# Optimization experiments

Measured on AMD Instinct MI355X. Metric: run time of the kernel, lower is better.

## Reference

```python
import jax, jax.numpy as jnp
from jax import lax
import numpy as np


def _conv3d(x, W, b, stride=1, pad=1):
    y = lax.conv_general_dilated(x, W, (stride,) * 3, [(pad, pad)] * 3,
                                 dimension_numbers=('NCDHW', 'OIDHW', 'NCDHW'))
    return y + b[None, :, None, None, None]


def _deconv3d(x, W, b):
    # PyTorch ConvTranspose3d(k=4, s=2, p=1) == conv with lhs_dilation=2,
    # per-side pad = k-1-p = 2, spatially flipped kernel; W is (Cin, Cout, 4,4,4).
    Wf = jnp.flip(W, axis=(2, 3, 4)).transpose(1, 0, 2, 3, 4)
    y = lax.conv_general_dilated(x, Wf, (1, 1, 1), [(2, 2)] * 3,
                                 lhs_dilation=(2, 2, 2),
                                 dimension_numbers=('NCDHW', 'OIDHW', 'NCDHW'))
    return y + b[None, :, None, None, None]


def _inorm(x, eps=1e-5):
    # InstanceNorm3d (affine=False): normalize per (B, C) over spatial dims
    m = jnp.mean(x, axis=(2, 3, 4), keepdims=True)
    v = jnp.var(x, axis=(2, 3, 4), keepdims=True)
    return (x - m) * lax.rsqrt(v + eps)


def _leaky(x):
    return jnp.where(x >= 0, x, 0.1 * x)


def _cblock(x, W, b, stride=1):
    return _leaky(_inorm(_conv3d(x, W, b, stride)))


def _cost_volume(f1, f2, r=2):
    # Faithful to the original pad/mul/crop loop:
    # cost[shift][p] = mean_c f1[c, p] * f2[c, p + shift], zero-padded OOB.
    B, C, D, H, W = f1.shape
    f2p = jnp.pad(f2, ((0, 0), (0, 0), (r, r), (r, r), (r, r)))
    cv = [jnp.mean(f1 * f2p[:, :, r + v:r + v + D, r + h:r + h + H, r + d:r + d + W], axis=1)
          for v in range(-r, r + 1)
          for h in range(-r, r + 1)
          for d in range(-r, r + 1)]
    return jnp.stack(cv, axis=1)  # (B, (2r+1)^3 = 125, D, H, W)


def _warp(img, flow):
    # SpatialTransformation: dense 3D warp, trilinear sample at grid + flow,
    # coordinates clamped to the volume border.
    B, C, D, H, W = img.shape
    gd, gh, gw = jnp.meshgrid(jnp.arange(D, dtype=img.dtype),
                              jnp.arange(H, dtype=img.dtype),
                              jnp.arange(W, dtype=img.dtype), indexing='ij')
    cd = jnp.clip(gd[None] + flow[:, 0], 0.0, D - 1.0)
    ch = jnp.clip(gh[None] + flow[:, 1], 0.0, H - 1.0)
    cw = jnp.clip(gw[None] + flow[:, 2], 0.0, W - 1.0)

    def samp_b(imb, d, h, w):
        return jax.vmap(lambda c: jax.scipy.ndimage.map_coordinates(
            c, [d, h, w], order=1, mode='nearest'))(imb)

    return jax.vmap(samp_b)(img, cd, ch, cw)


def _forward(atlas, target, W_ct, b_ct, W1a, b1a, W1aa, b1aa, W1b, b1b,
             W2a, b2a, W2aa, b2aa, W2b, b2b,
             W20, b20, Wpf2, bpf2, Wd2, bd2, Wuf2, buf2,
             W10, b10, Wpf1, bpf1, Wd1, bd1, Wuf1, buf1,
             W00, b00, Wpf0, bpf0, Wd0, bd0):
    # modality='CT' (shared CT encoder), G=True, contrastive=False path
    im2 = _cblock(atlas, W_ct, b_ct, stride=2)
    im1 = _cblock(target, W_ct, b_ct, stride=2)
    c11 = _cblock(_cblock(_cblock(im1, W1a, b1a, 2), W1aa, b1aa), W1b, b1b)
    c21 = _cblock(_cblock(_cblock(im2, W1a, b1a, 2), W1aa, b1aa), W1b, b1b)
    c12 = _cblock(_cblock(_cblock(c11, W2a, b2a, 2), W2aa, b2aa), W2b, b2b)
    c22 = _cblock(_cblock(_cblock(c21, W2a, b2a, 2), W2aa, b2aa), W2b, b2b)

    x = _leaky(_cost_volume(c12, c22))
    x = _cblock(x, W20, b20)
    flow2 = _conv3d(x, Wpf2, bpf2)
    up_flow2 = _deconv3d(flow2, Wd2, bd2)
    up_feat2 = _deconv3d(x, Wuf2, buf2)

    warp1 = _warp(c21, up_flow2)
    corr1 = _leaky(_cost_volume(c11, warp1))
    x = jnp.concatenate((corr1, c11, up_flow2, up_feat2), axis=1)  # 125+16+3+3=147
    x = _cblock(x, W10, b10)
    flow1 = _conv3d(x, Wpf1, bpf1)
    up_flow1 = _deconv3d(flow1, Wd1, bd1)
    up_feat1 = _deconv3d(x, Wuf1, buf1)

    warp0 = _warp(im2, up_flow1)
    corr0 = _leaky(_cost_volume(im1, warp0))
    x = jnp.concatenate((corr0, im1, up_flow1, up_feat1), axis=1)  # 125+4+3+64=196
    x = _cblock(x, W00, b00)
    flow0 = _conv3d(x, Wpf0, bpf0)
    flow = _deconv3d(flow0, Wd0, bd0)
    return flow, c22, c12


def setup_inputs() -> dict:
    ks = jax.random.split(jax.random.key(0), 24)

    def w(i, shape):
        fan_in = int(np.prod(shape[1:]))
        return jax.random.normal(ks[i], shape, jnp.float32) * np.float32(np.sqrt(2.0 / fan_in))

    z = lambda n: jnp.zeros((n,), jnp.float32)
    S = 128
    return {
        'atlas': jax.random.normal(ks[0], (1, 1, S, S, S), jnp.float32),
        'target': jax.random.normal(ks[1], (1, 1, S, S, S), jnp.float32),
        'W_ct': w(2, (4, 1, 3, 3, 3)), 'b_ct': z(4),
        'W1a': w(3, (16, 4, 3, 3, 3)), 'b1a': z(16),
        'W1aa': w(4, (16, 16, 3, 3, 3)), 'b1aa': z(16),
        'W1b': w(5, (16, 16, 3, 3, 3)), 'b1b': z(16),
        'W2a': w(6, (32, 16, 3, 3, 3)), 'b2a': z(32),
        'W2aa': w(7, (32, 32, 3, 3, 3)), 'b2aa': z(32),
        'W2b': w(8, (32, 32, 3, 3, 3)), 'b2b': z(32),
        'W20': w(9, (32, 125, 3, 3, 3)), 'b20': z(32),
        'Wpf2': w(10, (3, 32, 3, 3, 3)) * 0.1, 'bpf2': z(3),
        'Wd2': w(11, (3, 3, 4, 4, 4)), 'bd2': z(3),
        'Wuf2': w(12, (32, 3, 4, 4, 4)), 'buf2': z(3),
        'W10': w(13, (32, 147, 3, 3, 3)), 'b10': z(32),
        'Wpf1': w(14, (3, 32, 3, 3, 3)) * 0.1, 'bpf1': z(3),
        'Wd1': w(15, (3, 3, 4, 4, 4)), 'bd1': z(3),
        'Wuf1': w(16, (32, 64, 4, 4, 4)), 'buf1': z(64),
        'W00': w(17, (32, 196, 3, 3, 3)), 'b00': z(32),
        'Wpf0': w(18, (3, 32, 3, 3, 3)) * 0.1, 'bpf0': z(3),
        'Wd0': w(19, (3, 3, 4, 4, 4)), 'bd0': z(3),
    }


def reference(atlas, target, W_ct, b_ct, W1a, b1a, W1aa, b1aa, W1b, b1b,
              W2a, b2a, W2aa, b2aa, W2b, b2b,
              W20, b20, Wpf2, bpf2, Wd2, bd2, Wuf2, buf2,
              W10, b10, Wpf1, bpf1, Wd1, bd1, Wuf1, buf1,
              W00, b00, Wpf0, bpf0, Wd0, bd0):
    return _forward(atlas, target, W_ct, b_ct, W1a, b1a, W1aa, b1aa, W1b, b1b,
                    W2a, b2a, W2aa, b2aa, W2b, b2b,
                    W20, b20, Wpf2, bpf2, Wd2, bd2, Wuf2, buf2,
                    W10, b10, Wpf1, bpf1, Wd1, bd1, Wuf1, buf1,
                    W00, b00, Wpf0, bpf0, Wd0, bd0)
```

## Files before the change

kernel.cpp:

```cpp
#include <hip/hip_runtime.h>
#include <cstddef>
#include <cstdint>

#define DIVUP(a,b) (((a)+(b)-1)/(b))

typedef __attribute__((ext_vector_type(8))) short short8;
typedef __attribute__((ext_vector_type(4))) float f32x4;

__device__ __forceinline__ ushort f2bf(float f) {
    union { float f; uint32_t u; } v; v.f = f;
    uint32_t r = v.u + 0x7fffu + ((v.u >> 16) & 1u);
    return (ushort)(r >> 16);
}

struct SwzB { int x, y, z; };
__device__ __forceinline__ SwzB swz_block() {
    int gx = gridDim.x, gy = gridDim.y;
    int n = gx * gy * gridDim.z;
    int lin = blockIdx.x + gx * (blockIdx.y + gy * blockIdx.z);
    if ((n & 7) == 0)
        lin = (lin & 7) * (n >> 3) + (lin >> 3);
    SwzB s;
    s.x = lin % gx;
    int t = lin / gx;
    s.y = t % gy;
    s.z = t / gy;
    return s;
}

template<int COUT, int STRIDE>
__global__ __launch_bounds__(256)
void conv3x3_k(const float* __restrict__ in0, const float* __restrict__ in1,
               const float* __restrict__ wgt, const float* __restrict__ bias,
               float* __restrict__ out, float* __restrict__ stats,
               int Cin, int D, int H, int W, int nz, long out_bs, int st_bs)
{
    constexpr int TD = 4, TH = 8, TW = 8;
    constexpr int ID = 2 * TD + 1, IH = 2 * TH + 1, IW = 2 * TW + 1;
    __shared__ float tile[ID * IH * IW];
    const int b = blockIdx.z / nz, zb = blockIdx.z % nz;
    const float* in = b ? in1 : in0;
    out += (long)b * out_bs;
    if (stats) stats += 2 * st_bs * b;
    const int Do = D / STRIDE, Ho = H / STRIDE, Wo = W / STRIDE;
    const int tid = threadIdx.x;
    const int tw = tid & 7, th = (tid >> 3) & 7, td = tid >> 6;
    const int ow0 = blockIdx.x * TW, oh0 = blockIdx.y * TH, od0 = zb * TD;
    const int iw0 = ow0 * STRIDE - 1, ih0 = oh0 * STRIDE - 1, id0 = od0 * STRIDE - 1;
    const size_t HWs = (size_t)H * W;

    float acc[COUT];
#pragma unroll
    for (int i = 0; i < COUT; i++) acc[i] = 0.f;

    for (int c = 0; c < Cin; ++c) {
        const float* inc = in + (size_t)c * D * HWs;
        for (int i = tid; i < ID * IH * IW; i += 256) {
            int lw = i % IW, lh = (i / IW) % IH, ld = i / (IW * IH);
            int gw = iw0 + lw, gh = ih0 + lh, gd = id0 + ld;
            float v = 0.f;
            if ((unsigned)gw < (unsigned)W && (unsigned)gh < (unsigned)H &&
                (unsigned)gd < (unsigned)D)
                v = inc[(size_t)gd * HWs + (size_t)gh * W + gw];
            tile[i] = v;
        }
        __syncthreads();
        float r[27];
        const int bd = td * STRIDE, bh = th * STRIDE, bw = tw * STRIDE;
#pragma unroll
        for (int kd = 0; kd < 3; kd++)
#pragma unroll
            for (int kh = 0; kh < 3; kh++)
#pragma unroll
                for (int kw = 0; kw < 3; kw++)
                    r[kd * 9 + kh * 3 + kw] =
                        tile[(bd + kd) * (IH * IW) + (bh + kh) * IW + (bw + kw)];
#pragma unroll
        for (int oc = 0; oc < COUT; ++oc) {
            const float* wp = wgt + ((size_t)oc * Cin + c) * 27;
            float s = 0.f;
#pragma unroll
            for (int t = 0; t < 27; t++) s = fmaf(wp[t], r[t], s);
            acc[oc] += s;
        }
        __syncthreads();
    }
    const size_t So = (size_t)Do * Ho * Wo;
    const size_t sp = (size_t)(od0 + td) * Ho * Wo + (size_t)(oh0 + th) * Wo + (ow0 + tw);
#pragma unroll
    for (int oc = 0; oc < COUT; ++oc)
        out[(size_t)oc * So + sp] = acc[oc] + bias[oc];

    if (stats) {
        __syncthreads();
        float* sm = tile;
        const int wv = tid >> 6, l = tid & 63;
#pragma unroll
        for (int oc = 0; oc < COUT; ++oc) {
            float sv = acc[oc] + bias[oc];
            float sq = sv * sv;
#pragma unroll
            for (int o = 32; o > 0; o >>= 1) {
                sv += __shfl_down(sv, o, 64);
                sq += __shfl_down(sq, o, 64);
            }
            if (l == 0) { sm[(wv * COUT + oc) * 2] = sv; sm[(wv * COUT + oc) * 2 + 1] = sq; }
        }
        __syncthreads();
        if (tid < COUT) {
            float s = 0.f, s2 = 0.f;
#pragma unroll
            for (int w = 0; w < 4; ++w) {
                s += sm[(w * COUT + tid) * 2];
                s2 += sm[(w * COUT + tid) * 2 + 1];
            }
            atomicAdd(&stats[2 * tid], s);
            atomicAdd(&stats[2 * tid + 1], s2);
        }
    }
}

template<int CP, int NF, int STRIDE, int MW, int COUTR>
__global__ __launch_bounds__(MW * 64, (STRIDE == 1) ? 2 : 4)
void mconv_k(const ushort* __restrict__ xcl, const ushort* __restrict__ wp,
             const float* __restrict__ bias, float* __restrict__ outcf,
             float* __restrict__ stats, const ushort* __restrict__ zbuf,
             int D, int H, int W, int nz, long in_bs, long out_bs, int st_bs)
{
    constexpr int KC = CP / 32;
    constexpr int MF = (STRIDE == 1) ? 4 : 1;
    constexpr int TD = MW;
    constexpr int TWl = (STRIDE == 1) ? 8 : 4;
    constexpr int HD = (STRIDE == 1) ? TD + 2 : 2 * TD + 1;
    constexpr int HH = (STRIDE == 1) ? 10 : 9;
    constexpr int HWd = (STRIDE == 1) ? 10 : 9;
    constexpr int HALO = HD * HH * HWd;
    constexpr int NTH = MW * 64;
    constexpr int NIT = (HALO * 4 + NTH - 1) / NTH;
    constexpr int PITCH = (STRIDE == 1) ? 32 : 40;
    constexpr bool WLDS = (STRIDE == 1);
    constexpr int LDSZ_H = (STRIDE == 1) ? NIT * NTH * 8 : HALO * 40;
    constexpr int NITW = (9 * NF * 512 + NTH * 8 - 1) / (NTH * 8);
    constexpr int LDSZ_W = NITW * NTH * 8;
    constexpr int LDS_TOT = WLDS ? LDSZ_H + 2 * LDSZ_W : LDSZ_H;
    __shared__ __align__(16) ushort lds[LDS_TOT];

    const int tid = threadIdx.x;
    const int wv = tid >> 6, l = tid & 63;
    const SwzB sb = swz_block();
    const int b = sb.z / nz, zb = sb.z % nz;
    xcl += (long)b * in_bs;
    outcf += (long)b * out_bs;
    if (stats) stats += 2 * st_bs * b;
    const int od0 = zb * TD, oh0 = sb.y * ((STRIDE == 1) ? 8 : 4),
              ow0 = sb.x * TWl;
    const int id0 = od0 * STRIDE - 1, ih0 = oh0 * STRIDE - 1, iw0 = ow0 * STRIDE - 1;

    f32x4 acc[MF][NF];
#pragma unroll
    for (int mf = 0; mf < MF; mf++)
#pragma unroll
        for (int nf = 0; nf < NF; nf++) acc[mf][nf] = f32x4{0.f, 0.f, 0.f, 0.f};

    auto woff = [&](int kc, int kd, int kh, int kw, int nf) -> size_t {
        return ((((size_t)(kc * 3 + kd) * 3 + kh) * 3 + kw) * NF + nf) << 9;
    };

    if constexpr (WLDS) {
        ushort* const hab = lds;
        ushort* const wbA = lds + LDSZ_H;
        ushort* const wbB = lds + LDSZ_H + LDSZ_W;

        auto hstage = [&](int kc) {
#pragma unroll
            for (int it = 0; it < NIT; ++it) {
                int idx = it * NTH + tid;
                int pt = idx >> 2, part = idx & 3;
                int lw = pt % HWd, lh = (pt / HWd) % HH, ld = pt / (HWd * HH);
                int gx = iw0 + lw, gy = ih0 + lh, gz = id0 + ld;
                const ushort* src = zbuf;
                if (pt < HALO && (unsigned)gx < (unsigned)W &&
                    (unsigned)gy < (unsigned)H && (unsigned)gz < (unsigned)D)
                    src = xcl + (size_t)((gz * H + gy) * W + gx) * CP + part * 8;
                __builtin_amdgcn_global_load_lds(
                    (const __attribute__((address_space(1))) uint32_t*)(src + kc * 32),
                    (__attribute__((address_space(3))) uint32_t*)
                        &hab[(size_t)(it * NTH + (wv << 6)) * 8],
                    16, 0, 0);
            }
        };
        auto wstage = [&](int kc, int kd, ushort* dst) {
#pragma unroll
            for (int it = 0; it < NITW; ++it) {
                int idx = it * NTH + tid;
                const ushort* src = (idx < 9 * NF * 64)
                    ? wp + ((size_t)(kc * 3 + kd) * 9 * NF * 512 + (size_t)idx * 8)
                    : zbuf;
                __builtin_amdgcn_global_load_lds(
                    (const __attribute__((address_space(1))) uint32_t*)src,
                    (__attribute__((address_space(3))) uint32_t*)
                        &dst[(size_t)(it * NTH + (wv << 6)) * 8],
                    16, 0, 0);
            }
        };
        auto compute = [&](int kd, const ushort* w) {
#pragma unroll
            for (int kw = 0; kw < 3; ++kw) {
                short8 af[9];
#pragma unroll
                for (int r = 0; r < 9; ++r)
                    af[r] = *reinterpret_cast<const short8*>(
                        &hab[((wv + kd) * (HH * HWd) +
                              (r + ((l >> 3) & 1)) * HWd + (l & 7) + kw) * PITCH +
                             ((l >> 4) << 3)]);
#pragma unroll
                for (int kh = 0; kh < 3; ++kh) {
                    short8 bf[NF];
#pragma unroll
                    for (int nf = 0; nf < NF; ++nf)
                        bf[nf] = *reinterpret_cast<const short8*>(
                            &w[(size_t)(((kh * 3 + kw) * NF) + nf) * 512 + (l << 3)]);
#pragma unroll
                    for (int mf = 0; mf < MF; ++mf)
#pragma unroll
                        for (int nf = 0; nf < NF; ++nf)
                            acc[mf][nf] = __builtin_amdgcn_mfma_f32_16x16x32_bf16(
                                af[2 * mf + kh], bf[nf], acc[mf][nf], 0, 0, 0);
                }
            }
        };

        for (int kc = 0; kc < KC; ++kc) {
            hstage(kc);
            wstage(kc, 0, wbA);
            __syncthreads();
            wstage(kc, 1, wbB);
            compute(0, wbA);
            __syncthreads();
            wstage(kc, 2, wbA);
            compute(1, wbB);
            __syncthreads();
            compute(2, wbA);
            __syncthreads();
        }
    } else {
        uint4 v[NIT];
        auto stage = [&](int kc) {
#pragma unroll
            for (int it = 0; it < NIT; ++it) {
                int idx = it * NTH + tid;
                uint4 t = {0u, 0u, 0u, 0u};
                if (idx < HALO * 4) {
                    int pt = idx >> 2, part = idx & 3;
                    int lw = pt % HWd, lh = (pt / HWd) % HH, ld = pt / (HWd * HH);
                    int gx = iw0 + lw, gy = ih0 + lh, gz = id0 + ld;
                    if ((unsigned)gx < (unsigned)W && (unsigned)gy < (unsigned)H &&
                        (unsigned)gz < (unsigned)D)
                        t = *reinterpret_cast<const uint4*>(
                            xcl + ((size_t)((gz * H + gy) * W + gx)) * CP + kc * 32 + part * 8);
                }
                v[it] = t;
            }
        };

        stage(0);
        for (int kc = 0; kc < KC; ++kc) {
            if (kc) __syncthreads();
#pragma unroll
            for (int it = 0; it < NIT; ++it) {
                int idx = it * NTH + tid;
                if (idx < HALO * 4)
                    *reinterpret_cast<uint4*>(&lds[(idx >> 2) * PITCH + (idx & 3) * 8]) = v[it];
            }
            __syncthreads();
            if (kc + 1 < KC) stage(kc + 1);
#pragma unroll
            for (int t = 0; t < 27; ++t) {
                const int kd = t / 9, kh = (t / 3) % 3, kw = t % 3;
                short8 bf[NF];
#pragma unroll
                for (int nf = 0; nf < NF; ++nf)
                    bf[nf] = *reinterpret_cast<const short8*>(
                        wp + woff(kc, kd, kh, kw, nf) + (l << 3));
                int bw = l & 3, bh = (l >> 2) & 3;
                int p_loc = (2 * wv + kd) * (HH * HWd) + (2 * bh + kh) * HWd + (2 * bw + kw);
                short8 afs = *reinterpret_cast<const short8*>(&lds[p_loc * PITCH + ((l >> 4) << 3)]);
#pragma unroll
                for (int nf = 0; nf < NF; ++nf)
                    acc[0][nf] = __builtin_amdgcn_mfma_f32_16x16x32_bf16(
                        afs, bf[nf], acc[0][nf], 0, 0, 0);
            }
        }
    }
    const int Do = D / STRIDE, Ho = H / STRIDE, Wo = W / STRIDE;
    const size_t So = (size_t)Do * Ho * Wo;
    float ps[NF], ps2[NF];
#pragma unroll
    for (int nf = 0; nf < NF; ++nf) { ps[nf] = 0.f; ps2[nf] = 0.f; }
#pragma unroll
    for (int nf = 0; nf < NF; ++nf) {
        int oc = nf * 16 + (l & 15);
        float bv = (oc < COUTR) ? bias[oc] : 0.f;
#pragma unroll
        for (int mf = 0; mf < MF; ++mf) {
#pragma unroll
            for (int r = 0; r < 4; ++r) {
                int q = ((l >> 4) << 2) + r;
                int bw, bh;
                if (STRIDE == 1) { bw = q & 7; bh = 2 * mf + (q >> 3); }
                else             { bw = q & 3; bh = (q >> 2) & 3; }
                int p = ((od0 + wv) * Ho + (oh0 + bh)) * Wo + (ow0 + bw);
                float val = acc[mf][nf][r] + bv;
                if (oc < COUTR) {
                    outcf[(size_t)oc * So + p] = val;
                    ps[nf] += val; ps2[nf] = fmaf(val, val, ps2[nf]);
                }
            }
        }
    }
    if (stats) {
        __syncthreads();
        float* sm = (float*)lds;
#pragma unroll
        for (int nf = 0; nf < NF; ++nf) {
            float s = ps[nf], s2 = ps2[nf];
            s += __shfl_down(s, 32, 64);  s2 += __shfl_down(s2, 32, 64);
            s += __shfl_down(s, 16, 64);  s2 += __shfl_down(s2, 16, 64);
            if (l < 16) {
                sm[((wv * NF + nf) * 16 + l) * 2] = s;
                sm[((wv * NF + nf) * 16 + l) * 2 + 1] = s2;
            }
        }
        __syncthreads();
        if (tid < NF * 16) {
            int nf = tid >> 4, c = tid & 15, oc = nf * 16 + c;
            if (oc < COUTR) {
                float s = 0.f, s2 = 0.f;
#pragma unroll
                for (int w = 0; w < MW; ++w) {
                    s += sm[((w * NF + nf) * 16 + c) * 2];
                    s2 += sm[((w * NF + nf) * 16 + c) * 2 + 1];
                }
                atomicAdd(&stats[2 * oc], s);
                atomicAdd(&stats[2 * oc + 1], s2);
            }
        }
    }
}

struct WTask { const float* src; void* dst; int kind, Cin, COUT, KC, coutr, base; };
struct WTab { WTask t[17]; int n; };

__global__ __launch_bounds__(256)
void wprep_k(WTab tab)
{
    int b = blockIdx.x, ti = 0;
    for (int i = 0; i < tab.n; ++i) if (b >= tab.t[i].base) ti = i;
    const WTask tk = tab.t[ti];
    int idx = (b - tk.base) * 256 + threadIdx.x;
    if (tk.kind == 0) {
        int NF = tk.COUT >> 4;
        int tot = 27 * tk.KC * NF * 512;
        if (idx >= tot) return;
        int j = idx & 7, l = (idx >> 3) & 63;
        int g = idx >> 9;
        int nf = g % NF; g /= NF;
        int kw = g % 3; g /= 3;
        int kh = g % 3; g /= 3;
        int kd = g % 3; int kc = g / 3;
        int t = kd * 9 + kh * 3 + kw;
        int oc = nf * 16 + (l & 15);
        int c = kc * 32 + ((l >> 4) << 3) + j;
        float v = (c < tk.Cin && oc < tk.coutr)
                      ? tk.src[((size_t)oc * tk.Cin + c) * 27 + t] : 0.f;
        ((ushort*)tk.dst)[idx] = f2bf(v);
    } else if (tk.kind == 1) {
        int NF = tk.KC;
        int tot = 8 * 8 * NF * 512;
        if (idx >= tot) return;
        int j = idx & 7, l = (idx >> 3) & 63;
        int g = idx >> 9;
        int nf = g % NF; g /= NF;
        int t = g % 8; int pp = g / 8;
        int oc = nf * 16 + (l & 15);
        int c = ((l >> 4) << 3) + j;
        int kd_ = (t >> 2) & 1, kh_ = (t >> 1) & 1, kw_ = t & 1;
        int pd = (pp >> 2) & 1, ph = (pp >> 1) & 1, pw = pp & 1;
        int kd = 3 - pd - 2 * kd_, kh = 3 - ph - 2 * kh_, kw = 3 - pw - 2 * kw_;
        float v = (oc < tk.COUT)
                      ? tk.src[(size_t)(c * tk.COUT + oc) * 64 + kd * 16 + kh * 4 + kw] : 0.f;
        ((ushort*)tk.dst)[idx] = f2bf(v);
    } else {
        int tot = tk.Cin * tk.COUT * 64;
        if (idx >= tot) return;
        int k = idx & 63; int oc = (idx >> 6) % tk.COUT; int c = (idx >> 6) / tk.COUT;
        ((float*)tk.dst)[((size_t)c * 64 + k) * tk.COUT + oc] = tk.src[idx];
    }
}

template<int NF>
__global__ __launch_bounds__(256)
void mdeconv_k(const ushort* __restrict__ xcl, const ushort* __restrict__ wpd,
               const float* __restrict__ bias, ushort* __restrict__ outcl,
               int c0, int CPo, int Si)
{
    constexpr int HD = 5, HH = 9, HWd = 9, HALO = HD * HH * HWd;
    constexpr int PITCH = 32;
    __shared__ __align__(16) ushort lds[HALO * PITCH];
    const int tid = threadIdx.x, wv = tid >> 6, l = tid & 63;
    const SwzB sb = swz_block();
    const int pp = sb.z & 7, tz = sb.z >> 3;
    const int pd = (pp >> 2) & 1, ph = (pp >> 1) & 1, pw = pp & 1;
    const int oz0 = tz * 4, oy0 = sb.y * 8, ox0 = sb.x * 8;
    const int iz0 = oz0 + pd - 1, iy0 = oy0 + ph - 1, ix0 = ox0 + pw - 1;

    for (int idx = tid; idx < HALO * 4; idx += 256) {
        int pt = idx >> 2, part = idx & 3;
        int lw = pt % HWd, lh = (pt / HWd) % HH, ld = pt / (HWd * HH);
        int gx = ix0 + lw, gy = iy0 + lh, gz = iz0 + ld;
        uint4 t = {0u, 0u, 0u, 0u};
        if ((unsigned)gx < (unsigned)Si && (unsigned)gy < (unsigned)Si &&
            (unsigned)gz < (unsigned)Si)
            t = *reinterpret_cast<const uint4*>(
                xcl + ((size_t)((gz * Si + gy) * Si + gx)) * 32 + part * 8);
        *reinterpret_cast<uint4*>(&lds[pt * PITCH + part * 8]) = t;
    }
    __syncthreads();

    f32x4 acc[4][NF];
#pragma unroll
    for (int mf = 0; mf < 4; mf++)
#pragma unroll
        for (int nf = 0; nf < NF; nf++) acc[mf][nf] = f32x4{0.f, 0.f, 0.f, 0.f};

#pragma unroll
    for (int kd = 0; kd < 2; ++kd) {
#pragma unroll
        for (int kw = 0; kw < 2; ++kw) {
            short8 af[8];
#pragma unroll
            for (int r = 0; r < 8; ++r)
                af[r] = *reinterpret_cast<const short8*>(
                    &lds[((wv + kd) * (HH * HWd) + (r + ((l >> 3) & 1)) * HWd +
                          (l & 7) + kw) * PITCH + ((l >> 4) << 3)]);
#pragma unroll
            for (int kh = 0; kh < 2; ++kh) {
                const int t = kd * 4 + kh * 2 + kw;
                short8 bf[NF];
#pragma unroll
                for (int nf = 0; nf < NF; ++nf)
                    bf[nf] = *reinterpret_cast<const short8*>(
                        wpd + (((size_t)(pp * 8 + t) * NF + nf) << 9) + (l << 3));
#pragma unroll
                for (int mf = 0; mf < 4; ++mf)
#pragma unroll
                    for (int nf = 0; nf < NF; ++nf)
                        acc[mf][nf] = __builtin_amdgcn_mfma_f32_16x16x32_bf16(
                            af[2 * mf + kh], bf[nf], acc[mf][nf], 0, 0, 0);
            }
        }
    }
    const int Do = 2 * Si;
#pragma unroll
    for (int nf = 0; nf < NF; ++nf) {
        int oc = nf * 16 + (l & 15);
        float bv = bias[oc];
#pragma unroll
        for (int mf = 0; mf < 4; ++mf) {
#pragma unroll
            for (int r = 0; r < 4; ++r) {
                int q = ((l >> 4) << 2) + r;
                int bw = q & 7, bh = 2 * mf + (q >> 3);
                int oD = 2 * (oz0 + wv) + pd, oH = 2 * (oy0 + bh) + ph, oW = 2 * (ox0 + bw) + pw;
                outcl[(size_t)((oD * Do + oH) * Do + oW) * CPo + c0 + oc] =
                    f2bf(acc[mf][nf][r] + bv);
            }
        }
    }
}

template<int CIN>
__global__ __launch_bounds__(256)
void dctn_k(const float* __restrict__ in, const float* __restrict__ wt,
            const float* __restrict__ bias, float* __restrict__ outcf,
            ushort* __restrict__ outcl, int c0, int CPo, int Si)
{
    const int Do = 2 * Si;
    const size_t So = (size_t)Do * Do * Do, ni = (size_t)Si * Si * Si;
    size_t p = (size_t)blockIdx.x * 256 + threadIdx.x;
    if (p >= So) return;
    int oxW = (int)(p % Do), oyH = (int)((p / Do) % Do), ozD = (int)(p / ((size_t)Do * Do));
    int pw = oxW & 1, ph = oyH & 1, pd = ozD & 1;
    int xb = oxW >> 1, yb = oyH >> 1, zb = ozD >> 1;
    float acc[3] = {0.f, 0.f, 0.f};
    for (int c = 0; c < CIN; ++c) {
        const float* inc = in + (size_t)c * ni;
        const float* wc = wt + (size_t)c * 64 * 3;
#pragma unroll
        for (int jd = 0; jd < 2; jd++) {
            int iz = zb + pd - jd; if ((unsigned)iz >= (unsigned)Si) continue;
            int kd = 1 - pd + 2 * jd;
#pragma unroll
            for (int jh = 0; jh < 2; jh++) {
                int iy = yb + ph - jh; if ((unsigned)iy >= (unsigned)Si) continue;
                int kh = 1 - ph + 2 * jh;
#pragma unroll
                for (int jw = 0; jw < 2; jw++) {
                    int ix = xb + pw - jw; if ((unsigned)ix >= (unsigned)Si) continue;
                    int kw = 1 - pw + 2 * jw;
                    float v = inc[((size_t)iz * Si + iy) * Si + ix];
                    const float* wr = wc + (size_t)((kd * 4 + kh) * 4 + kw) * 3;
                    acc[0] = fmaf(wr[0], v, acc[0]);
                    acc[1] = fmaf(wr[1], v, acc[1]);
                    acc[2] = fmaf(wr[2], v, acc[2]);
                }
            }
        }
    }
#pragma unroll
    for (int oc = 0; oc < 3; ++oc) {
        float o = acc[oc] + bias[oc];
        if (outcf) outcf[(size_t)oc * So + p] = o;
        if (outcl) outcl[p * CPo + c0 + oc] = f2bf(o);
    }
}

__global__ __launch_bounds__(256)
void inorm_apply_k(const float* __restrict__ x, const float* __restrict__ stats,
                   float* __restrict__ y, size_t S, float invS,
                   ushort* __restrict__ ycl, int CP, int Cper, long ycl_bs,
                   float* __restrict__ yclf, int CPf, int Cf)
{
    int c = blockIdx.y;
    float sum = stats[2 * c], ss = stats[2 * c + 1];
    float m = sum * invS;
    float r = rsqrtf(fmaxf(ss * invS - m * m, 0.f) + 1e-5f);
    size_t i = (size_t)blockIdx.x * 256 + threadIdx.x;
    if (i >= S) return;
    float v = (x[(size_t)c * S + i] - m) * r;
    v = v >= 0.f ? v : 0.1f * v;
    y[(size_t)c * S + i] = v;
    if (ycl) {
        int b = c / Cper, cl = c - b * Cper;
        ycl[(long)b * ycl_bs + (long)i * CP + cl] = f2bf(v);
    }
    if (yclf && c < Cf)
        yclf[i * (size_t)CPf + c] = v;
}

template<int C, int CP, int COPYC>
__global__ __launch_bounds__(256)
void costvolw_k(const float* __restrict__ f1, const float* __restrict__ f2,
                ushort* __restrict__ outcl, int D, int H, int W)
{
    const size_t S = (size_t)D * H * W;
    size_t p = (size_t)blockIdx.x * 4 + (threadIdx.x >> 6);
    if (p >= S) return;
    const int l = threadIdx.x & 63;
    int x = (int)(p % W); int y = (int)((p / W) % H); int z = (int)(p / ((size_t)W * H));
    float a[C];
#pragma unroll
    for (int c = 0; c < C; c++) a[c] = f1[(size_t)c * S + p];
    const float inv = 1.f / C;
    ushort* op = outcl + p * CP;
#pragma unroll
    for (int rep = 0; rep < 2; rep++) {
        int s = l + rep * 64;
        if (s < 125) {
            int v = s / 25 - 2, h = (s / 5) % 5 - 2, d = s % 5 - 2;
            int zz = z + v, yy = y + h, xx = x + d;
            float acc = 0.f;
            if ((unsigned)zz < (unsigned)D && (unsigned)yy < (unsigned)H &&
                (unsigned)xx < (unsigned)W) {
                size_t q = ((size_t)zz * H + yy) * (size_t)W + xx;
#pragma unroll
                for (int c = 0; c < C; c++) acc = fmaf(a[c], f2[(size_t)c * S + q], acc);
            }
            acc *= inv;
            op[s] = f2bf(acc >= 0.f ? acc : 0.1f * acc);
        }
    }
    if (COPYC && l < C)
        op[125 + l] = f2bf(f1[(size_t)l * S + p]);
}

template<int C, int CP, int NP>
__global__ __launch_bounds__(256)
void costvolcl_k(const float* __restrict__ f1cl, const float* __restrict__ f2cl,
                 ushort* __restrict__ outcl, int D, int H, int W)
{
    const size_t S = (size_t)D * H * W;
    size_t p0 = ((size_t)blockIdx.x * 4 + (threadIdx.x >> 6)) * NP;
    if (p0 >= S) return;
    const int l = threadIdx.x & 63;
    float a[NP][C];
#pragma unroll
    for (int pp = 0; pp < NP; pp++)
#pragma unroll
        for (int c4 = 0; c4 < C / 4; c4++) {
            float4 t = *reinterpret_cast<const float4*>(&f1cl[(p0 + pp) * C + c4 * 4]);
            a[pp][c4 * 4 + 0] = t.x; a[pp][c4 * 4 + 1] = t.y;
            a[pp][c4 * 4 + 2] = t.z; a[pp][c4 * 4 + 3] = t.w;
        }
    const float inv = 1.f / C;
#pragma unroll
    for (int rep = 0; rep < 2; rep++) {
        int s = l + rep * 64;
        int v = s / 25 - 2, h = (s / 5) % 5 - 2, d = s % 5 - 2;
        bool sv = s < 125;
#pragma unroll
        for (int pp = 0; pp < NP; pp++) {
            size_t p = p0 + pp;
            int x = (int)(p % W), y = (int)((p / W) % H), z = (int)(p / ((size_t)W * H));
            int zz = z + v, yy = y + h, xx = x + d;
            float acc = 0.f;
            if (sv && (unsigned)zz < (unsigned)D && (unsigned)yy < (unsigned)H &&
                (unsigned)xx < (unsigned)W) {
                size_t q = ((size_t)zz * H + yy) * (size_t)W + xx;
#pragma unroll
                for (int c4 = 0; c4 < C / 4; c4++) {
                    float4 b = *reinterpret_cast<const float4*>(&f2cl[q * C + c4 * 4]);
                    acc = fmaf(a[pp][c4 * 4 + 0], b.x, acc);
                    acc = fmaf(a[pp][c4 * 4 + 1], b.y, acc);
                    acc = fmaf(a[pp][c4 * 4 + 2], b.z, acc);
                    acc = fmaf(a[pp][c4 * 4 + 3], b.w, acc);
                }
            }
            if (sv) {
                acc *= inv;
                outcl[p * CP + s] = f2bf(acc >= 0.f ? acc : 0.1f * acc);
            }
        }
    }
    if (l < C) {
#pragma unroll
        for (int pp = 0; pp < NP; pp++)
            outcl[(p0 + pp) * CP + 125 + l] = f2bf(f1cl[(p0 + pp) * C + l]);
    }
}

template<int C>
__global__ __launch_bounds__(256)
void warpcl_k(const float* __restrict__ img, const float* __restrict__ flow,
              float* __restrict__ outcl, int D, int H, int W)
{
    const size_t S = (size_t)D * H * W;
    size_t p = (size_t)blockIdx.x * 256 + threadIdx.x;
    if (p >= S) return;
    int x = (int)(p % W); int y = (int)((p / W) % H); int z = (int)(p / ((size_t)W * H));
    float cd = fminf(fmaxf((float)z + flow[p], 0.f), (float)(D - 1));
    float ch = fminf(fmaxf((float)y + flow[S + p], 0.f), (float)(H - 1));
    float cw = fminf(fmaxf((float)x + flow[2 * S + p], 0.f), (float)(W - 1));
    int d0 = (int)cd, h0 = (int)ch, w0 = (int)cw;
    float fd = cd - d0, fh = ch - h0, fw = cw - w0;
    int d1 = min(d0 + 1, D - 1), h1 = min(h0 + 1, H - 1), w1 = min(w0 + 1, W - 1);
    size_t i000 = ((size_t)d0 * H + h0) * W + w0, i001 = ((size_t)d0 * H + h0) * W + w1;
    size_t i010 = ((size_t)d0 * H + h1) * W + w0, i011 = ((size_t)d0 * H + h1) * W + w1;
    size_t i100 = ((size_t)d1 * H + h0) * W + w0, i101 = ((size_t)d1 * H + h0) * W + w1;
    size_t i110 = ((size_t)d1 * H + h1) * W + w0, i111 = ((size_t)d1 * H + h1) * W + w1;
    float w000 = (1 - fd) * (1 - fh) * (1 - fw), w001 = (1 - fd) * (1 - fh) * fw;
    float w010 = (1 - fd) * fh * (1 - fw),       w011 = (1 - fd) * fh * fw;
    float w100 = fd * (1 - fh) * (1 - fw),       w101 = fd * (1 - fh) * fw;
    float w110 = fd * fh * (1 - fw),             w111 = fd * fh * fw;
#pragma unroll
    for (int c4 = 0; c4 < C / 4; c4++) {
        float4 r;
        float* rr = reinterpret_cast<float*>(&r);
#pragma unroll
        for (int j = 0; j < 4; j++) {
            const float* ic = img + (size_t)(c4 * 4 + j) * S;
            rr[j] = w000 * ic[i000] + w001 * ic[i001] + w010 * ic[i010] + w011 * ic[i011]
                  + w100 * ic[i100] + w101 * ic[i101] + w110 * ic[i110] + w111 * ic[i111];
        }
        *reinterpret_cast<float4*>(&outcl[p * C + c4 * 4]) = r;
    }
}

static void apply(hipStream_t st, float* x, int C, size_t S, const float* stats,
                  ushort* ycl, int CP, int Cper, long ycl_bs,
                  float* yclf = nullptr, int CPf = 0, int Cf = 0)
{
    dim3 g((unsigned)DIVUP(S, 256), C);
    inorm_apply_k<<<g, 256, 0, st>>>(x, stats, x, S, 1.0f / (float)S, ycl, CP, Cper, ycl_bs,
                                     yclf, CPf, Cf);
}

extern "C" void kernel_launch(void* const* d_in, const int* in_sizes, int n_in,
                              void* d_out, int out_size, void* d_ws, size_t ws_size,
                              hipStream_t st)
{
    (void)in_sizes; (void)n_in; (void)out_size; (void)ws_size;
    const float* atlas  = (const float*)d_in[0];
    const float* target = (const float*)d_in[1];
    const float *W_ct = (const float*)d_in[2],  *b_ct = (const float*)d_in[3];
    const float *W1a  = (const float*)d_in[4],  *b1a  = (const float*)d_in[5];
    const float *W1aa = (const float*)d_in[6],  *b1aa = (const float*)d_in[7];
    const float *W1b  = (const float*)d_in[8],  *b1b  = (const float*)d_in[9];
    const float *W2a  = (const float*)d_in[10], *b2a  = (const float*)d_in[11];
    const float *W2aa = (const float*)d_in[12], *b2aa = (const float*)d_in[13];
    const float *W2b  = (const float*)d_in[14], *b2b  = (const float*)d_in[15];
    const float *W20  = (const float*)d_in[16], *b20  = (const float*)d_in[17];
    const float *Wpf2 = (const float*)d_in[18], *bpf2 = (const float*)d_in[19];
    const float *Wd2  = (const float*)d_in[20], *bd2  = (const float*)d_in[21];
    const float *Wuf2 = (const float*)d_in[22], *buf2 = (const float*)d_in[23];
    const float *W10  = (const float*)d_in[24], *b10  = (const float*)d_in[25];
    const float *Wpf1 = (const float*)d_in[26], *bpf1 = (const float*)d_in[27];
    const float *Wd1  = (const float*)d_in[28], *bd1  = (const float*)d_in[29];
    const float *Wuf1 = (const float*)d_in[30], *buf1 = (const float*)d_in[31];
    const float *W00  = (const float*)d_in[32], *b00  = (const float*)d_in[33];
    const float *Wpf0 = (const float*)d_in[34], *bpf0 = (const float*)d_in[35];
    const float *Wd0  = (const float*)d_in[36], *bd0  = (const float*)d_in[37];

    const size_t S128 = 128u * 128 * 128, S64 = 64u * 64 * 64, S32 = 32u * 32 * 32, S16 = 16u * 16 * 16;

    char* base = (char*)d_ws;
    size_t off = 0;
    auto AF = [&](size_t n) { off = (off + 255) & ~(size_t)255; float* p = (float*)(base + off); off += n * 4; return p; };
    auto AH = [&](size_t n) { off = (off + 255) & ~(size_t)255; ushort* p = (ushort*)(base + off); off += n * 2; return p; };

    ushort* wp1a  = AH(13824);  ushort* wp1aa = AH(13824); ushort* wp1b = AH(13824);
    ushort* wp2a  = AH(27648);  ushort* wp2aa = AH(27648); ushort* wp2b = AH(27648);
    ushort* wp20  = AH(110592); ushort* wp10 = AH(138240); ushort* wp00 = AH(193536);
    ushort* wpf2  = AH(13824);  ushort* wpf1 = AH(13824);  ushort* wpf0 = AH(13824);
    ushort* wpd_uf1 = AH(131072);
    float* wt_uf2 = AF(6144);
    float* wt_d2  = AF(576);    float* wt_d1 = AF(576);    float* wt_d0 = AF(576);
    float* stats = AF(1024);
    ushort* zbuf = AH(1024);
    float* im12 = AF(8 * S64);
    float* im1 = im12; float* im2 = im12 + 4 * S64;
    float* im1clf = AF(4 * S64);
    float* warp0clf = AF(4 * S64);
    float* c11clf = AF(16 * S32);
    float* warp1clf = AF(16 * S32);
    float* A1   = AF(32 * S32); ushort* A1cl = AH(2 * S32 * 32);
    float* B1   = AF(32 * S32); ushort* B1cl = AH(2 * S32 * 32);
    float* c1121 = AF(32 * S32); ushort* c1121cl = AH(2 * S32 * 32);
    float* c11 = c1121; float* c21 = c1121 + 16 * S32;
    float* A2   = AF(64 * S16); ushort* A2cl = AH(2 * S16 * 32);
    float* B2   = AF(64 * S16); ushort* B2cl = AH(2 * S16 * 32);
    ushort* cv2cl = AH(S16 * 128);
    float* x20  = AF(32 * S16); ushort* x20cl = AH(S16 * 32);
    float* flow2 = AF(3 * S16); float* upflow2 = AF(3 * S32);
    ushort* x147cl = AH(S32 * 160);
    float* x10  = AF(32 * S32); ushort* x10cl = AH(S32 * 32);
    float* flow1 = AF(3 * S32); float* upflow1 = AF(3 * S64);
    ushort* x196cl = AH(S64 * 224);
    float* x00  = AF(32 * S64); float* flow0 = AF(3 * S64);

    ushort* im12cl = x196cl;
    ushort* x00cl = x196cl;

    float* outF = (float*)d_out;
    float* c22o = outF + 3 * S128;
    float* c12o = c22o + 32 * S16;

    const int ST_IM=0, ST_A1=8, ST_B1=40, ST_C1=72, ST_A2=104, ST_B2=168, ST_C2=232,
              ST_X20=296, ST_X10=328, ST_X00=360;
    auto SP = [&](int o) { return stats + 2 * o; };
    hipMemsetAsync(stats, 0, 4096, st);
    hipMemsetAsync(zbuf, 0, 2048, st);

    WTab tab; int nb = 0, ti = 0;
    auto addw = [&](const float* s, void* d, int kind, int Cin, int COUT, int KC, int coutr) {
        int tot = (kind == 0) ? 27 * KC * (COUT >> 4) * 512
                 : (kind == 1) ? 8 * 8 * KC * 512 : Cin * COUT * 64;
        tab.t[ti] = WTask{s, d, kind, Cin, COUT, KC, coutr, nb};
        nb += DIVUP(tot, 256); ti++;
    };
    addw(W1a,  wp1a,  0,  4, 16, 1, 16);
    addw(W1aa, wp1aa, 0, 16, 16, 1, 16);
    addw(W1b,  wp1b,  0, 16, 16, 1, 16);
    addw(W2a,  wp2a,  0, 16, 32, 1, 32);
    addw(W2aa, wp2aa, 0, 32, 32, 1, 32);
    addw(W2b,  wp2b,  0, 32, 32, 1, 32);
    addw(W20,  wp20,  0, 125, 32, 4, 32);
    addw(W10,  wp10,  0, 147, 32, 5, 32);
    addw(W00,  wp00,  0, 196, 32, 7, 32);
    addw(Wpf2, wpf2,  0, 32, 16, 1, 3);
    addw(Wpf1, wpf1,  0, 32, 16, 1, 3);
    addw(Wpf0, wpf0,  0, 32, 16, 1, 3);
    addw(Wuf1, wpd_uf1, 1, 32, 64, 4, 64);
    addw(Wuf2, wt_uf2, 2, 32, 3, 0, 3);
    addw(Wd2,  wt_d2,  2, 3, 3, 0, 3);
    addw(Wd1,  wt_d1,  2, 3, 3, 0, 3);
    addw(Wd0,  wt_d0,  2, 3, 3, 0, 3);
    tab.n = ti;
    wprep_k<<<nb, 256, 0, st>>>(tab);

    conv3x3_k<4, 2><<<dim3(8, 8, 32), 256, 0, st>>>(target, atlas, W_ct, b_ct, im12,
                                                    SP(ST_IM), 1, 128, 128, 128,
                                                    16, (long)(4 * S64), 4);
    apply(st, im12, 8, S64, SP(ST_IM), im12cl, 32, 4, (long)(32 * S64), im1clf, 4, 4);

    mconv_k<32, 1, 2, 4, 16><<<dim3(8, 8, 16), 256, 0, st>>>(im12cl, wp1a, b1a, A1, SP(ST_A1),
        zbuf, 64, 64, 64, 8, (long)(32 * S64), (long)(16 * S32), 16);
    apply(st, A1, 32, S32, SP(ST_A1), A1cl, 32, 16, (long)(S32 * 32));
    mconv_k<32, 1, 1, 2, 16><<<dim3(4, 4, 32), 128, 0, st>>>(A1cl, wp1aa, b1aa, B1, SP(ST_B1),
        zbuf, 32, 32, 32, 16, (long)(S32 * 32), (long)(16 * S32), 16);
    apply(st, B1, 32, S32, SP(ST_B1), B1cl, 32, 16, (long)(S32 * 32));
    mconv_k<32, 1, 1, 2, 16><<<dim3(4, 4, 32), 128, 0, st>>>(B1cl, wp1b, b1b, c1121, SP(ST_C1),
        zbuf, 32, 32, 32, 16, (long)(S32 * 32), (long)(16 * S32), 16);
    apply(st, c1121, 32, S32, SP(ST_C1), c1121cl, 32, 16, (long)(S32 * 32), c11clf, 16, 16);

    mconv_k<32, 2, 2, 4, 32><<<dim3(4, 4, 8), 256, 0, st>>>(c1121cl, wp2a, b2a, A2, SP(ST_A2),
        zbuf, 32, 32, 32, 4, (long)(S32 * 32), (long)(32 * S16), 32);
    apply(st, A2, 64, S16, SP(ST_A2), A2cl, 32, 32, (long)(S16 * 32));
    mconv_k<32, 2, 1, 2, 32><<<dim3(2, 2, 16), 128, 0, st>>>(A2cl, wp2aa, b2aa, B2, SP(ST_B2),
        zbuf, 16, 16, 16, 8, (long)(S16 * 32), (long)(32 * S16), 32);
    apply(st, B2, 64, S16, SP(ST_B2), B2cl, 32, 32, (long)(S16 * 32));
    mconv_k<32, 2, 1, 2, 32><<<dim3(2, 2, 16), 128, 0, st>>>(B2cl, wp2b, b2b, c12o, SP(ST_C2),
        zbuf, 16, 16, 16, 8, (long)(S16 * 32), (long)(c22o - c12o), 32);
    apply(st, c12o, 32, S16, SP(ST_C2), nullptr, 0, 32, 0);
    apply(st, c22o, 32, S16, SP(ST_C2 + 32), nullptr, 0, 32, 0);

    costvolw_k<32, 128, 0><<<DIVUP(S16, 4), 256, 0, st>>>(c12o, c22o, cv2cl, 16, 16, 16);
    mconv_k<128, 2, 1, 2, 32><<<dim3(2, 2, 8), 128, 0, st>>>(cv2cl, wp20, b20, x20, SP(ST_X20),
        zbuf, 16, 16, 16, 8, 0, 0, 0);
    apply(st, x20, 32, S16, SP(ST_X20), x20cl, 32, 32, 0);
    mconv_k<32, 1, 1, 2, 3><<<dim3(2, 2, 8), 128, 0, st>>>(x20cl, wpf2, bpf2, flow2, nullptr,
        zbuf, 16, 16, 16, 8, 0, 0, 0);
    dctn_k<3><<<DIVUP(8 * S16, 256), 256, 0, st>>>(flow2, wt_d2, bd2, upflow2, x147cl, 141, 160, 16);
    dctn_k<32><<<DIVUP(8 * S16, 256), 256, 0, st>>>(x20, wt_uf2, buf2, nullptr, x147cl, 144, 160, 16);

    warpcl_k<16><<<DIVUP(S32, 256), 256, 0, st>>>(c21, upflow2, warp1clf, 32, 32, 32);
    costvolcl_k<16, 160, 2><<<(unsigned)(S32 / 8), 256, 0, st>>>(c11clf, warp1clf, x147cl,
                                                                 32, 32, 32);
    mconv_k<160, 2, 1, 2, 32><<<dim3(4, 4, 16), 128, 0, st>>>(x147cl, wp10, b10, x10, SP(ST_X10),
        zbuf, 32, 32, 32, 16, 0, 0, 0);
    apply(st, x10, 32, S32, SP(ST_X10), x10cl, 32, 32, 0);
    mconv_k<32, 1, 1, 2, 3><<<dim3(4, 4, 16), 128, 0, st>>>(x10cl, wpf1, bpf1, flow1, nullptr,
        zbuf, 32, 32, 32, 16, 0, 0, 0);
    dctn_k<3><<<DIVUP(8 * S32, 256), 256, 0, st>>>(flow1, wt_d1, bd1, upflow1, x196cl, 129, 224, 32);
    mdeconv_k<4><<<dim3(4, 4, 64), 256, 0, st>>>(x10cl, wpd_uf1, buf1, x196cl, 132, 224, 32);

    warpcl_k<4><<<DIVUP(S64, 256), 256, 0, st>>>(im2, upflow1, warp0clf, 64, 64, 64);
    costvolcl_k<4, 224, 4><<<(unsigned)(S64 / 16), 256, 0, st>>>(im1clf, warp0clf, x196cl,
                                                                 64, 64, 64);
    mconv_k<224, 2, 1, 4, 32><<<dim3(8, 8, 16), 256, 0, st>>>(x196cl, wp00, b00, x00, SP(ST_X00),
        zbuf, 64, 64, 64, 16, 0, 0, 0);
    apply(st, x00, 32, S64, SP(ST_X00), x00cl, 32, 32, 0);
    mconv_k<32, 1, 1, 4, 3><<<dim3(8, 8, 16), 256, 0, st>>>(x00cl, wpf0, bpf0, flow0, nullptr,
        zbuf, 64, 64, 64, 16, 0, 0, 0);
    dctn_k<3><<<DIVUP(S128, 256), 256, 0, st>>>(flow0, wt_d0, bd0, outF, nullptr, 0, 0, 64);
}
```

Baseline: 869.5 us.

## Stage stride-2 conv and deconv weights in LDS; use direct conv for first layer

The stride-2 MFMA conv path and the transposed-conv kernel now copy their weight slices into shared memory with async global-to-LDS loads. The inner loops then read B fragments from LDS instead of issuing repeated global loads. Separately, the first encoder conv (4 input channels) now calls the direct conv3x3 kernel on the fp32 inputs. This drops the padded 32-channel channels-last repack and its weight prepack. The cost is larger shared-memory footprints, which may lower occupancy, and the direct kernel may be slower for this layer than the MFMA one.

```diff
diff --git a/kernel.cpp b/kernel.cpp
--- a/kernel.cpp
+++ b/kernel.cpp
@@ -138,11 +138,12 @@
     constexpr int NTH = MW * 64;
     constexpr int NIT = (HALO * 4 + NTH - 1) / NTH;
     constexpr int PITCH = (STRIDE == 1) ? 32 : 40;
-    constexpr bool WLDS = (STRIDE == 1);
     constexpr int LDSZ_H = (STRIDE == 1) ? NIT * NTH * 8 : HALO * 40;
     constexpr int NITW = (9 * NF * 512 + NTH * 8 - 1) / (NTH * 8);
+    constexpr int NITW2 = (27 * NF * 512 + NTH * 8 - 1) / (NTH * 8);
     constexpr int LDSZ_W = NITW * NTH * 8;
-    constexpr int LDS_TOT = WLDS ? LDSZ_H + 2 * LDSZ_W : LDSZ_H;
+    constexpr int LDSZ_W2 = NITW2 * NTH * 8;
+    constexpr int LDS_TOT = (STRIDE == 1) ? LDSZ_H + 2 * LDSZ_W : LDSZ_H + LDSZ_W2;
     __shared__ __align__(16) ushort lds[LDS_TOT];
 
     const int tid = threadIdx.x;
@@ -162,11 +163,7 @@
 #pragma unroll
         for (int nf = 0; nf < NF; nf++) acc[mf][nf] = f32x4{0.f, 0.f, 0.f, 0.f};
 
-    auto woff = [&](int kc, int kd, int kh, int kw, int nf) -> size_t {
-        return ((((size_t)(kc * 3 + kd) * 3 + kh) * 3 + kw) * NF + nf) << 9;
-    };
-
-    if constexpr (WLDS) {
+    if constexpr (STRIDE == 1) {
         ushort* const hab = lds;
         ushort* const wbA = lds + LDSZ_H;
         ushort* const wbB = lds + LDSZ_H + LDSZ_W;
@@ -244,6 +241,7 @@
             __syncthreads();
         }
     } else {
+        ushort* const wlds = lds + LDSZ_H;
         uint4 v[NIT];
         auto stage = [&](int kc) {
 #pragma unroll
@@ -262,6 +260,20 @@
                 v[it] = t;
             }
         };
+        auto wstage2 = [&](int kc) {
+#pragma unroll
+            for (int it = 0; it < NITW2; ++it) {
+                int idx = it * NTH + tid;
+                const ushort* src = (idx < 27 * NF * 64)
+                    ? wp + ((size_t)kc * 27 * NF * 512 + (size_t)idx * 8)
+                    : zbuf;
+                __builtin_amdgcn_global_load_lds(
+                    (const __attribute__((address_space(1))) uint32_t*)src,
+                    (__attribute__((address_space(3))) uint32_t*)
+                        &wlds[(size_t)(it * NTH + (wv << 6)) * 8],
+                    16, 0, 0);
+            }
+        };
 
         stage(0);
         for (int kc = 0; kc < KC; ++kc) {
@@ -272,6 +284,7 @@
                 if (idx < HALO * 4)
                     *reinterpret_cast<uint4*>(&lds[(idx >> 2) * PITCH + (idx & 3) * 8]) = v[it];
             }
+            wstage2(kc);
             __syncthreads();
             if (kc + 1 < KC) stage(kc + 1);
 #pragma unroll
@@ -281,7 +294,7 @@
 #pragma unroll
                 for (int nf = 0; nf < NF; ++nf)
                     bf[nf] = *reinterpret_cast<const short8*>(
-                        wp + woff(kc, kd, kh, kw, nf) + (l << 3));
+                        &wlds[(size_t)(t * NF + nf) * 512 + (l << 3)]);
                 int bw = l & 3, bh = (l >> 2) & 3;
                 int p_loc = (2 * wv + kd) * (HH * HWd) + (2 * bh + kh) * HWd + (2 * bw + kw);
                 short8 afs = *reinterpret_cast<const short8*>(&lds[p_loc * PITCH + ((l >> 4) << 3)]);
@@ -402,11 +415,14 @@
 __global__ __launch_bounds__(256)
 void mdeconv_k(const ushort* __restrict__ xcl, const ushort* __restrict__ wpd,
                const float* __restrict__ bias, ushort* __restrict__ outcl,
-               int c0, int CPo, int Si)
+               const ushort* __restrict__ zbuf, int c0, int CPo, int Si)
 {
     constexpr int HD = 5, HH = 9, HWd = 9, HALO = HD * HH * HWd;
     constexpr int PITCH = 32;
-    __shared__ __align__(16) ushort lds[HALO * PITCH];
+    constexpr int WCH = 8 * NF * 512;
+    constexpr int NITW = (WCH / 8 + 255) / 256;
+    __shared__ __align__(16) ushort lds[HALO * PITCH + NITW * 256 * 8];
+    ushort* const wlds = lds + HALO * PITCH;
     const int tid = threadIdx.x, wv = tid >> 6, l = tid & 63;
     const SwzB sb = swz_block();
     const int pp = sb.z & 7, tz = sb.z >> 3;
@@ -414,6 +430,17 @@
     const int oz0 = tz * 4, oy0 = sb.y * 8, ox0 = sb.x * 8;
     const int iz0 = oz0 + pd - 1, iy0 = oy0 + ph - 1, ix0 = ox0 + pw - 1;
 
+#pragma unroll
+    for (int it = 0; it < NITW; ++it) {
+        int idx = it * 256 + tid;
+        const ushort* src = (idx < WCH / 8)
+            ? wpd + (size_t)pp * WCH + (size_t)idx * 8 : zbuf;
+        __builtin_amdgcn_global_load_lds(
+            (const __attribute__((address_space(1))) uint32_t*)src,
+            (__attribute__((address_space(3))) uint32_t*)
+                &wlds[(size_t)(it * 256 + (wv << 6)) * 8],
+            16, 0, 0);
+    }
     for (int idx = tid; idx < HALO * 4; idx += 256) {
         int pt = idx >> 2, part = idx & 3;
         int lw = pt % HWd, lh = (pt / HWd) % HH, ld = pt / (HWd * HH);
@@ -450,7 +477,7 @@
 #pragma unroll
                 for (int nf = 0; nf < NF; ++nf)
                     bf[nf] = *reinterpret_cast<const short8*>(
-                        wpd + (((size_t)(pp * 8 + t) * NF + nf) << 9) + (l << 3));
+                        &wlds[(size_t)(t * NF + nf) * 512 + (l << 3)]);
 #pragma unroll
                 for (int mf = 0; mf < 4; ++mf)
 #pragma unroll
@@ -718,8 +745,8 @@
     auto AF = [&](size_t n) { off = (off + 255) & ~(size_t)255; float* p = (float*)(base + off); off += n * 4; return p; };
     auto AH = [&](size_t n) { off = (off + 255) & ~(size_t)255; ushort* p = (ushort*)(base + off); off += n * 2; return p; };
 
-    ushort* wp1a  = AH(13824);  ushort* wp1aa = AH(13824); ushort* wp1b = AH(13824);
-    ushort* wp2a  = AH(27648);  ushort* wp2aa = AH(27648); ushort* wp2b = AH(27648);
+    ushort* wp1aa = AH(13824); ushort* wp1b = AH(13824);
+    ushort* wp2a  = AH(27648); ushort* wp2aa = AH(27648); ushort* wp2b = AH(27648);
     ushort* wp20  = AH(110592); ushort* wp10 = AH(138240); ushort* wp00 = AH(193536);
     ushort* wpf2  = AH(13824);  ushort* wpf1 = AH(13824);  ushort* wpf0 = AH(13824);
     ushort* wpd_uf1 = AH(131072);
@@ -748,7 +775,6 @@
     ushort* x196cl = AH(S64 * 224);
     float* x00  = AF(32 * S64); float* flow0 = AF(3 * S64);
 
-    ushort* im12cl = x196cl;
     ushort* x00cl = x196cl;
 
     float* outF = (float*)d_out;
@@ -768,7 +794,6 @@
         tab.t[ti] = WTask{s, d, kind, Cin, COUT, KC, coutr, nb};
         nb += DIVUP(tot, 256); ti++;
     };
-    addw(W1a,  wp1a,  0,  4, 16, 1, 16);
     addw(W1aa, wp1aa, 0, 16, 16, 1, 16);
     addw(W1b,  wp1b,  0, 16, 16, 1, 16);
     addw(W2a,  wp2a,  0, 16, 32, 1, 32);
@@ -791,10 +816,11 @@
     conv3x3_k<4, 2><<<dim3(8, 8, 32), 256, 0, st>>>(target, atlas, W_ct, b_ct, im12,
                                                     SP(ST_IM), 1, 128, 128, 128,
                                                     16, (long)(4 * S64), 4);
-    apply(st, im12, 8, S64, SP(ST_IM), im12cl, 32, 4, (long)(32 * S64), im1clf, 4, 4);
-
-    mconv_k<32, 1, 2, 4, 16><<<dim3(8, 8, 16), 256, 0, st>>>(im12cl, wp1a, b1a, A1, SP(ST_A1),
-        zbuf, 64, 64, 64, 8, (long)(32 * S64), (long)(16 * S32), 16);
+    apply(st, im12, 8, S64, SP(ST_IM), nullptr, 0, 4, 0, im1clf, 4, 4);
+
+    conv3x3_k<16, 2><<<dim3(4, 4, 16), 256, 0, st>>>(im1, im2, W1a, b1a, A1,
+                                                     SP(ST_A1), 4, 64, 64, 64,
+                                                     8, (long)(16 * S32), 16);
     apply(st, A1, 32, S32, SP(ST_A1), A1cl, 32, 16, (long)(S32 * 32));
     mconv_k<32, 1, 1, 2, 16><<<dim3(4, 4, 32), 128, 0, st>>>(A1cl, wp1aa, b1aa, B1, SP(ST_B1),
         zbuf, 32, 32, 32, 16, (long)(S32 * 32), (long)(16 * S32), 16);
@@ -832,7 +858,7 @@
     mconv_k<32, 1, 1, 2, 3><<<dim3(4, 4, 16), 128, 0, st>>>(x10cl, wpf1, bpf1, flow1, nullptr,
         zbuf, 32, 32, 32, 16, 0, 0, 0);
     dctn_k<3><<<DIVUP(8 * S32, 256), 256, 0, st>>>(flow1, wt_d1, bd1, upflow1, x196cl, 129, 224, 32);
-    mdeconv_k<4><<<dim3(4, 4, 64), 256, 0, st>>>(x10cl, wpd_uf1, buf1, x196cl, 132, 224, 32);
+    mdeconv_k<4><<<dim3(4, 4, 64), 256, 0, st>>>(x10cl, wpd_uf1, buf1, x196cl, zbuf, 132, 224, 32);
 
     warpcl_k<4><<<DIVUP(S64, 256), 256, 0, st>>>(im2, upflow1, warp0clf, 64, 64, 64);
     costvolcl_k<4, 224, 4><<<(unsigned)(S64 / 16), 256, 0, st>>>(im1clf, warp0clf, x196cl,
```

New measurement: 890.9 us. 1.02x slower.
